# Optimization experiments

Measured on AMD Instinct MI355X. Metric: run time of the kernel, lower is better.

The kernel has to match this reference:

```python
import jax, jax.numpy as jnp
import numpy as np

HIDDEN = 64
DEPTH = 4  # 4 tanh layers + final linear


def _mlp(x, Ws, bs):
    # x: [..., 3] -> [..., 1]; weights stored as (in, out)
    h = x
    for W, b in zip(Ws[:-1], bs[:-1]):
        h = jnp.tanh(h @ W + b)
    return h @ Ws[-1] + bs[-1]


def setup_inputs() -> dict:
    key = jax.random.key(0)
    N = 262144
    dims = [3, HIDDEN, HIDDEN, HIDDEN, HIDDEN, 1]
    ks = jax.random.split(key, 2 * len(dims) + 3)
    inp = {}
    inp["x_data"] = jax.random.normal(ks[0], (N, 3), dtype=jnp.float32)
    inp["y_data"] = jax.random.normal(ks[1], (N, 1), dtype=jnp.float32)
    inp["x_phys"] = jax.random.normal(ks[2], (N, 3), dtype=jnp.float32)
    for i in range(5):
        fan_in = dims[i]
        bound = 1.0 / np.sqrt(fan_in)
        inp[f"W{i}"] = jax.random.uniform(ks[3 + 2 * i], (dims[i], dims[i + 1]),
                                          minval=-bound, maxval=bound, dtype=jnp.float32)
        inp[f"b{i}"] = jax.random.uniform(ks[4 + 2 * i], (dims[i + 1],),
                                          minval=-bound, maxval=bound, dtype=jnp.float32)
    inp["log_lambda"] = jnp.array([-2.0], dtype=jnp.float32)
    inp["log_alpha"] = jnp.array([-4.0], dtype=jnp.float32)
    return inp


def reference(x_data, y_data, x_phys,
              W0, b0, W1, b1, W2, b2, W3, b3, W4, b4,
              log_lambda, log_alpha):
    Ws = (W0, W1, W2, W3, W4)
    bs = (b0, b1, b2, b3, b4)
    alpha = jnp.exp(log_alpha)[0]
    lam = jnp.exp(log_lambda)[0]

    # data loss
    y_pred = _mlp(x_data, Ws, bs)  # [N,1]
    data_loss = jnp.mean((y_pred - y_data) ** 2)

    # PDE residual: dT/dt - alpha * (d2T/dx2 + d2T/dy2)
    def scalar_net(x):  # x: [3] -> scalar
        return _mlp(x, Ws, bs)[0]

    g = jax.grad(scalar_net)
    grads = jax.vmap(g)(x_phys)  # [N,3]
    dT_dt = grads[:, 2]

    e0 = jnp.array([1.0, 0.0, 0.0], dtype=x_phys.dtype)
    e1 = jnp.array([0.0, 1.0, 0.0], dtype=x_phys.dtype)

    def second_xy(x):
        # forward-over-reverse: Hessian columns for x and y directions
        _, hx = jax.jvp(g, (x,), (e0,))
        _, hy = jax.jvp(g, (x,), (e1,))
        return hx[0], hy[1]

    d2T_dx2, d2T_dy2 = jax.vmap(second_xy)(x_phys)  # each [N]

    residual = dT_dt - alpha * (d2T_dx2 + d2T_dy2)
    pde_loss = jnp.mean(residual ** 2)
    total_loss = data_loss + lam * pde_loss
    return total_loss, data_loss, pde_loss, alpha, lam
```

## Files before the change

kernel.cpp:

```cpp
#include <hip/hip_runtime.h>
#include <math.h>

#define NSAMP 262144
#define NW 4
#define BLK 256
#define PB 1024
#define DB 512
#define GRID (PB + DB)

#define SB_MASK 0x120

typedef _Float16 f16x8 __attribute__((ext_vector_type(8)));
typedef _Float16 f16x4 __attribute__((ext_vector_type(4)));
typedef __fp16   fp16x2 __attribute__((ext_vector_type(2)));
typedef float    f32x4 __attribute__((ext_vector_type(4)));
typedef float    f32x2 __attribute__((ext_vector_type(2)));

#define NCH 4

#define TWO_LOG2E 2.8853900817779268f

__device__ __forceinline__ f32x2 lo2(f32x4 v) { return __builtin_shufflevector(v, v, 0, 1); }
__device__ __forceinline__ f32x2 hi2(f32x4 v) { return __builtin_shufflevector(v, v, 2, 3); }
__device__ __forceinline__ f32x2 splat2(float s) { f32x2 v; v.x = s; v.y = s; return v; }

__device__ __forceinline__ f32x2 fast_tanh2(f32x2 x) {
    f32x2 t = x * splat2(TWO_LOG2E);
    f32x2 e;
    e.x = __builtin_amdgcn_exp2f(t.x);
    e.y = __builtin_amdgcn_exp2f(t.y);
    f32x2 d = e + splat2(1.0f);
    f32x2 rc;
    rc.x = __builtin_amdgcn_rcpf(d.x);
    rc.y = __builtin_amdgcn_rcpf(d.y);
    return splat2(1.0f) - splat2(2.0f) * rc;
}

__device__ __forceinline__ void phys_half(f32x2 z0, f32x2 z1, f32x2 z2, f32x2 z3,
                                          f32x2 alpha2, f32x2 (&h)[NCH])
{
    f32x2 a    = fast_tanh2(z0);
    f32x2 ap   = splat2(1.0f) - a * a;
    f32x2 napp = (a * ap) * alpha2;
    h[0] = a;
    h[1] = ap * z1;
    h[2] = ap * z2;
    f32x2 s = z1 * z1 + z2 * z2;
    h[3] = ap * z3 + napp * s;
}

__device__ __forceinline__ f16x4 pkpair(f32x2 lo, f32x2 hi) {
    union { f16x4 v; fp16x2 h[2]; } u;
    u.h[0] = __builtin_amdgcn_cvt_pkrtz(lo.x, lo.y);
    u.h[1] = __builtin_amdgcn_cvt_pkrtz(hi.x, hi.y);
    return u.v;
}

__device__ __forceinline__ void set_half(f16x8& dst, f16x4 v, int hi) {
    if (hi == 0) { dst[0] = v[0]; dst[1] = v[1]; dst[2] = v[2]; dst[3] = v[3]; }
    else         { dst[4] = v[0]; dst[5] = v[1]; dst[6] = v[2]; dst[7] = v[3]; }
}

__device__ __forceinline__ double shfl_xor_d(double v, int m) {
    union { double d; int i[2]; } u; u.d = v;
    u.i[0] = __shfl_xor(u.i[0], m, 64);
    u.i[1] = __shfl_xor(u.i[1], m, 64);
    return u.d;
}

template<bool DATA>
__device__ __forceinline__ void pw(const f32x4* acc, f16x4* out, f32x2 alpha2)
{
    if (DATA) {
        #pragma unroll
        for (int c = 0; c < NCH; c++)
            out[c] = pkpair(fast_tanh2(lo2(acc[c])), fast_tanh2(hi2(acc[c])));
    } else {
        f32x2 hlo[NCH], hhi[NCH];
        phys_half(lo2(acc[0]), lo2(acc[1]), lo2(acc[2]), lo2(acc[3]), alpha2, hlo);
        phys_half(hi2(acc[0]), hi2(acc[1]), hi2(acc[2]), hi2(acc[3]), alpha2, hhi);
        #pragma unroll
        for (int c = 0; c < NCH; c++) out[c] = pkpair(hlo[c], hhi[c]);
    }
}

template<bool DATA>
__device__ __forceinline__ void layer_mfma(
    const _Float16* sWA, const float (*sB)[64],
    int l, int rt, int q, int n, const f16x8 (&bf)[NCH][2], f32x4 (&acc)[NCH])
{
    const f32x4 z4 = {0.f, 0.f, 0.f, 0.f};
    f16x8 a0k = *(const f16x8*)&sWA[((((l * 4 + rt) * 2 + 0) * 4 + q) * 16 + n) * 8];
    f16x8 a1k = *(const f16x8*)&sWA[((((l * 4 + rt) * 2 + 1) * 4 + q) * 16 + n) * 8];
    f32x4 bias = *(const f32x4*)&sB[l + 1][rt * 16 + q * 4];
    #pragma unroll
    for (int c = 0; c < NCH; c++) {
        f32x4 cin = (DATA || c == 0) ? bias : z4;
        acc[c] = __builtin_amdgcn_mfma_f32_16x16x32_f16(a0k, bf[c][0], cin, 0, 0, 0);
        acc[c] = __builtin_amdgcn_mfma_f32_16x16x32_f16(a1k, bf[c][1], acc[c], 0, 0, 0);
    }
}

template<bool DATA>
__device__ __forceinline__ void hidden_layer(
    const _Float16* sWA, const float (*sB)[64],
    int l, int q, int n, const f16x8 (&bin)[NCH][2], f16x8 (&bout)[NCH][2], f32x2 alpha2)
{
    #pragma unroll
    for (int rt = 0; rt < 4; rt++) {
        f32x4 acc[NCH];
        layer_mfma<DATA>(sWA, sB, l, rt, q, n, bin, acc);
        f16x4 t6[NCH];
        pw<DATA>(acc, t6, alpha2);
        #pragma unroll
        for (int c = 0; c < NCH; c++) set_half(bout[c][rt >> 1], t6[c], rt & 1);
        __builtin_amdgcn_sched_barrier(SB_MASK);
    }
}

template<bool DATA>
__device__ __forceinline__ double run_mode(
    const float* __restrict__ xd, const float* __restrict__ yd,
    const float* __restrict__ xp, float alpha,
    const _Float16* sWA, const f16x8 (&a0r)[4],
    const float (*sB)[64], const float* sW4, float b4,
    int q, int n, int wstart, int wstride)
{
    const f16x8 zf = {0, 0, 0, 0, 0, 0, 0, 0};
    const f32x4 z4 = {0.f, 0.f, 0.f, 0.f};
    const f32x2 alpha2 = splat2(2.0f * alpha);

    const int NIT = DATA ? (NSAMP / (16 * NCH)) : (NSAMP / 16);
    double dacc = 0.0;

    for (int it = wstart; it < NIT; it += wstride) {
        f16x8 bfA[NCH][2], bfB[NCH][2];
        {
            f16x8 b0f[NCH];
            #pragma unroll
            for (int c = 0; c < NCH; c++) b0f[c] = zf;
            if (DATA) {
                if (q == 0) {
                    #pragma unroll
                    for (int c = 0; c < NCH; c++) {
                        int s = it * (16 * NCH) + c * 16 + n;
                        b0f[c][0] = (_Float16)xd[s * 3 + 0];
                        b0f[c][1] = (_Float16)xd[s * 3 + 1];
                        b0f[c][2] = (_Float16)xd[s * 3 + 2];
                    }
                }
            } else {
                if (q == 0) {
                    int s = it * 16 + n;
                    b0f[0][0] = (_Float16)xp[s * 3 + 0];
                    b0f[0][1] = (_Float16)xp[s * 3 + 1];
                    b0f[0][2] = (_Float16)xp[s * 3 + 2];
                    b0f[1][0] = (_Float16)1.0f;
                    b0f[2][1] = (_Float16)1.0f;
                    b0f[3][2] = (_Float16)1.0f;
                }
            }
            #pragma unroll
            for (int rt = 0; rt < 4; rt++) {
                f32x4 bias = *(const f32x4*)&sB[0][rt * 16 + q * 4];
                f32x4 acc[NCH];
                if (DATA) {
                    #pragma unroll
                    for (int c = 0; c < NCH; c++)
                        acc[c] = __builtin_amdgcn_mfma_f32_16x16x32_f16(a0r[rt], b0f[c], bias, 0, 0, 0);
                } else {
                    acc[0] = __builtin_amdgcn_mfma_f32_16x16x32_f16(a0r[rt], b0f[0], bias, 0, 0, 0);
                    #pragma unroll
                    for (int c = 1; c < NCH; c++)
                        acc[c] = __builtin_amdgcn_mfma_f32_16x16x32_f16(a0r[rt], b0f[c], z4, 0, 0, 0);
                }
                f16x4 t6[NCH];
                pw<DATA>(acc, t6, alpha2);
                #pragma unroll
                for (int c = 0; c < NCH; c++) set_half(bfA[c][rt >> 1], t6[c], rt & 1);
                __builtin_amdgcn_sched_barrier(SB_MASK);
            }
        }

        hidden_layer<DATA>(sWA, sB, 0, q, n, bfA, bfB, alpha2);
        hidden_layer<DATA>(sWA, sB, 1, q, n, bfB, bfA, alpha2);

        f32x2 t2[NCH];
        #pragma unroll
        for (int c = 0; c < NCH; c++) t2[c] = splat2(0.f);
        f32x2 tr2 = splat2(0.f);
        #pragma unroll
        for (int rt = 0; rt < 4; rt++) {
            f32x4 acc[NCH];
            layer_mfma<DATA>(sWA, sB, 2, rt, q, n, bfA, acc);
            f32x4 w4v = *(const f32x4*)&sW4[rt * 16 + q * 4];
            f32x2 wlo = lo2(w4v), whi = hi2(w4v);
            if (DATA) {
                #pragma unroll
                for (int c = 0; c < NCH; c++) {
                    t2[c] = t2[c] + wlo * fast_tanh2(lo2(acc[c]));
                    t2[c] = t2[c] + whi * fast_tanh2(hi2(acc[c]));
                }
            } else {
                f32x2 hlo[NCH], hhi[NCH];
                phys_half(lo2(acc[0]), lo2(acc[1]), lo2(acc[2]), lo2(acc[3]), alpha2, hlo);
                phys_half(hi2(acc[0]), hi2(acc[1]), hi2(acc[2]), hi2(acc[3]), alpha2, hhi);
                tr2 = tr2 + wlo * hlo[3];
                tr2 = tr2 + whi * hhi[3];
            }
        }

        if (DATA) {
            float t[NCH];
            #pragma unroll
            for (int c = 0; c < NCH; c++) {
                t[c] = t2[c].x + t2[c].y;
                t[c] += __shfl_xor(t[c], 16, 64);
                t[c] += __shfl_xor(t[c], 32, 64);
            }
            if (q == 0) {
                #pragma unroll
                for (int c = 0; c < NCH; c++) {
                    int s = it * (16 * NCH) + c * 16 + n;
                    float d = t[c] + b4 - yd[s];
                    dacc += (double)d * (double)d;
                }
            }
        } else {
            float tr = tr2.x + tr2.y;
            tr += __shfl_xor(tr, 16, 64);
            tr += __shfl_xor(tr, 32, 64);
            if (q == 0) dacc += (double)tr * (double)tr;
        }
    }
    return dacc;
}

__global__ __launch_bounds__(BLK)
__attribute__((amdgpu_waves_per_eu(2, 6)))
void fused_kernel(
    const float* __restrict__ xd, const float* __restrict__ yd, const float* __restrict__ xp,
    const float* __restrict__ W0, const float* __restrict__ b0,
    const float* __restrict__ W1, const float* __restrict__ b1,
    const float* __restrict__ W2, const float* __restrict__ b2,
    const float* __restrict__ W3, const float* __restrict__ b3,
    const float* __restrict__ W4, const float* __restrict__ b4,
    const float* __restrict__ log_alpha,
    double* __restrict__ accg)
{
    __shared__ __align__(16) _Float16 sWA[3 * 4 * 2 * 4 * 16 * 8];
    __shared__ __align__(16) float sB[4][64];
    __shared__ __align__(16) float sW4s[64];
    __shared__ float sb4;
    __shared__ double sRed[NW];

    const int tid = threadIdx.x;
    for (int idx = tid; idx < 3 * 4096; idx += BLK) {
        int l = idx >> 12, rem = idx & 4095, k = rem >> 6, m = rem & 63;
        const float* Ws = (l == 0) ? W1 : (l == 1) ? W2 : W3;
        int pk_ = (2 * (k >> 5) + ((k >> 2) & 1)) * 16 + ((k >> 3) & 3) * 4 + (k & 3);
        int rt = m >> 4, mlo = m & 15, kt = k >> 5, qq = (k >> 3) & 3, j = k & 7;
        sWA[((((l * 4 + rt) * 2 + kt) * 4 + qq) * 16 + mlo) * 8 + j] = (_Float16)Ws[pk_ * 64 + m];
    }
    for (int i = tid; i < 64; i += BLK) {
        sB[0][i] = b0[i]; sB[1][i] = b1[i]; sB[2][i] = b2[i]; sB[3][i] = b3[i];
        sW4s[i] = W4[i];
    }
    if (tid == 0) sb4 = b4[0];

    const int wave = tid >> 6, lane = tid & 63;
    const int q = lane >> 4, n = lane & 15;
    const float alpha = __expf(log_alpha[0]);

    f16x8 a0r[4];
    #pragma unroll
    for (int rt = 0; rt < 4; rt++) {
        f16x8 v = {0, 0, 0, 0, 0, 0, 0, 0};
        if (q == 0) {
            v[0] = (_Float16)W0[0 * 64 + rt * 16 + n];
            v[1] = (_Float16)W0[1 * 64 + rt * 16 + n];
            v[2] = (_Float16)W0[2 * 64 + rt * 16 + n];
        }
        a0r[rt] = v;
    }
    __syncthreads();

    double dacc;
    if (blockIdx.x < PB) {
        int ws = blockIdx.x * NW + wave;
        dacc = run_mode<false>(xd, yd, xp, alpha, sWA, a0r, sB, sW4s, sb4,
                               q, n, ws, PB * NW);
    } else {
        int ws = (blockIdx.x - PB) * NW + wave;
        dacc = run_mode<true>(xd, yd, xp, alpha, sWA, a0r, sB, sW4s, sb4,
                              q, n, ws, DB * NW);
    }
    #pragma unroll
    for (int m = 1; m < 64; m <<= 1) dacc = dacc + shfl_xor_d(dacc, m);
    if (lane == 0) sRed[wave] = dacc;
    __syncthreads();
    if (tid == 0)
        accg[blockIdx.x] = sRed[0] + sRed[1] + sRed[2] + sRed[3];
}

__global__ void finalize_kernel(const double* __restrict__ ws,
                                const float* __restrict__ log_lambda,
                                const float* __restrict__ log_alpha,
                                float* __restrict__ out)
{
    __shared__ double sp[256], sd[256];
    int tid = threadIdx.x;
    double pd = 0.0, dd = 0.0;
    for (int i = tid; i < PB; i += 256) pd += ws[i];
    for (int i = PB + tid; i < GRID; i += 256) dd += ws[i];
    sp[tid] = pd; sd[tid] = dd;
    __syncthreads();
    for (int s = 128; s > 0; s >>= 1) {
        if (tid < s) { sp[tid] += sp[tid + s]; sd[tid] += sd[tid + s]; }
        __syncthreads();
    }
    if (tid == 0) {
        float pde_loss  = (float)(sp[0] / (double)NSAMP);
        float data_loss = (float)(sd[0] / (double)NSAMP);
        float alpha = expf(log_alpha[0]);
        float lam   = expf(log_lambda[0]);
        out[0] = data_loss + lam * pde_loss;
        out[1] = data_loss;
        out[2] = pde_loss;
        out[3] = alpha;
        out[4] = lam;
    }
}

extern "C" void kernel_launch(void* const* d_in, const int* in_sizes, int n_in,
                              void* d_out, int out_size, void* d_ws, size_t ws_size,
                              hipStream_t stream) {
    const float* xd = (const float*)d_in[0];
    const float* yd = (const float*)d_in[1];
    const float* xp = (const float*)d_in[2];
    const float* W0 = (const float*)d_in[3];
    const float* b0 = (const float*)d_in[4];
    const float* W1 = (const float*)d_in[5];
    const float* b1 = (const float*)d_in[6];
    const float* W2 = (const float*)d_in[7];
    const float* b2 = (const float*)d_in[8];
    const float* W3 = (const float*)d_in[9];
    const float* b3 = (const float*)d_in[10];
    const float* W4 = (const float*)d_in[11];
    const float* b4 = (const float*)d_in[12];
    const float* log_lambda = (const float*)d_in[13];
    const float* log_alpha  = (const float*)d_in[14];
    float* out = (float*)d_out;
    double* acc = (double*)d_ws;

    fused_kernel<<<GRID, BLK, 0, stream>>>(xd, yd, xp, W0, b0, W1, b1, W2, b2, W3, b3,
                                           W4, b4, log_alpha, acc);
    finalize_kernel<<<1, 256, 0, stream>>>(acc, log_lambda, log_alpha, out);
}
```

Measured before the change: 150.3 us.

## Run physics and data passes in every wave with larger blocks

Replaces the split of blocks into dedicated physics and data blocks with a uniform grid of 1024 blocks of 8 waves. Each wave now runs the physics pass and then the data pass. The data pass uses 2 chunks instead of 4 to cut register pressure, and per-block partial sums are written as interleaved pairs. This is meant to balance load across waves and raise occupancy. The cost is doubling the number of template instantiations in one kernel, which may raise register use, and fewer chunks per data iteration reduce MFMA batching.

Result: no change. 151.6 us (+0.8%).

```diff
diff --git a/kernel.cpp b/kernel.cpp
--- a/kernel.cpp
+++ b/kernel.cpp
@@ -2,11 +2,10 @@
 #include <math.h>
 
 #define NSAMP 262144
-#define NW 4
-#define BLK 256
-#define PB 1024
-#define DB 512
-#define GRID (PB + DB)
+#define NW 8
+#define BLK 512
+#define GRID 1024
+#define TOTW (GRID * NW)
 
 #define SB_MASK 0x120
 
@@ -16,7 +15,7 @@
 typedef float    f32x4 __attribute__((ext_vector_type(4)));
 typedef float    f32x2 __attribute__((ext_vector_type(2)));
 
-#define NCH 4
+#define PCH 4
 
 #define TWO_LOG2E 2.8853900817779268f
 
@@ -37,7 +36,7 @@
 }
 
 __device__ __forceinline__ void phys_half(f32x2 z0, f32x2 z1, f32x2 z2, f32x2 z3,
-                                          f32x2 alpha2, f32x2 (&h)[NCH])
+                                          f32x2 alpha2, f32x2 (&h)[PCH])
 {
     f32x2 a    = fast_tanh2(z0);
     f32x2 ap   = splat2(1.0f) - a * a;
@@ -68,57 +67,57 @@
     return u.d;
 }
 
-template<bool DATA>
+template<bool DATA, int CH>
 __device__ __forceinline__ void pw(const f32x4* acc, f16x4* out, f32x2 alpha2)
 {
-    if (DATA) {
-        #pragma unroll
-        for (int c = 0; c < NCH; c++)
+    if constexpr (DATA) {
+        #pragma unroll
+        for (int c = 0; c < CH; c++)
             out[c] = pkpair(fast_tanh2(lo2(acc[c])), fast_tanh2(hi2(acc[c])));
     } else {
-        f32x2 hlo[NCH], hhi[NCH];
+        f32x2 hlo[PCH], hhi[PCH];
         phys_half(lo2(acc[0]), lo2(acc[1]), lo2(acc[2]), lo2(acc[3]), alpha2, hlo);
         phys_half(hi2(acc[0]), hi2(acc[1]), hi2(acc[2]), hi2(acc[3]), alpha2, hhi);
         #pragma unroll
-        for (int c = 0; c < NCH; c++) out[c] = pkpair(hlo[c], hhi[c]);
-    }
-}
-
-template<bool DATA>
+        for (int c = 0; c < CH; c++) out[c] = pkpair(hlo[c], hhi[c]);
+    }
+}
+
+template<bool DATA, int CH>
 __device__ __forceinline__ void layer_mfma(
     const _Float16* sWA, const float (*sB)[64],
-    int l, int rt, int q, int n, const f16x8 (&bf)[NCH][2], f32x4 (&acc)[NCH])
+    int l, int rt, int q, int n, const f16x8 (&bf)[CH][2], f32x4 (&acc)[CH])
 {
     const f32x4 z4 = {0.f, 0.f, 0.f, 0.f};
     f16x8 a0k = *(const f16x8*)&sWA[((((l * 4 + rt) * 2 + 0) * 4 + q) * 16 + n) * 8];
     f16x8 a1k = *(const f16x8*)&sWA[((((l * 4 + rt) * 2 + 1) * 4 + q) * 16 + n) * 8];
     f32x4 bias = *(const f32x4*)&sB[l + 1][rt * 16 + q * 4];
     #pragma unroll
-    for (int c = 0; c < NCH; c++) {
+    for (int c = 0; c < CH; c++) {
         f32x4 cin = (DATA || c == 0) ? bias : z4;
         acc[c] = __builtin_amdgcn_mfma_f32_16x16x32_f16(a0k, bf[c][0], cin, 0, 0, 0);
         acc[c] = __builtin_amdgcn_mfma_f32_16x16x32_f16(a1k, bf[c][1], acc[c], 0, 0, 0);
     }
 }
 
-template<bool DATA>
+template<bool DATA, int CH>
 __device__ __forceinline__ void hidden_layer(
     const _Float16* sWA, const float (*sB)[64],
-    int l, int q, int n, const f16x8 (&bin)[NCH][2], f16x8 (&bout)[NCH][2], f32x2 alpha2)
+    int l, int q, int n, const f16x8 (&bin)[CH][2], f16x8 (&bout)[CH][2], f32x2 alpha2)
 {
     #pragma unroll
     for (int rt = 0; rt < 4; rt++) {
-        f32x4 acc[NCH];
-        layer_mfma<DATA>(sWA, sB, l, rt, q, n, bin, acc);
-        f16x4 t6[NCH];
-        pw<DATA>(acc, t6, alpha2);
-        #pragma unroll
-        for (int c = 0; c < NCH; c++) set_half(bout[c][rt >> 1], t6[c], rt & 1);
+        f32x4 acc[CH];
+        layer_mfma<DATA, CH>(sWA, sB, l, rt, q, n, bin, acc);
+        f16x4 t6[CH];
+        pw<DATA, CH>(acc, t6, alpha2);
+        #pragma unroll
+        for (int c = 0; c < CH; c++) set_half(bout[c][rt >> 1], t6[c], rt & 1);
         __builtin_amdgcn_sched_barrier(SB_MASK);
     }
 }
 
-template<bool DATA>
+template<bool DATA, int CH>
 __device__ __forceinline__ double run_mode(
     const float* __restrict__ xd, const float* __restrict__ yd,
     const float* __restrict__ xp, float alpha,
@@ -130,20 +129,20 @@
     const f32x4 z4 = {0.f, 0.f, 0.f, 0.f};
     const f32x2 alpha2 = splat2(2.0f * alpha);
 
-    const int NIT = DATA ? (NSAMP / (16 * NCH)) : (NSAMP / 16);
+    const int NIT = DATA ? (NSAMP / (16 * CH)) : (NSAMP / 16);
     double dacc = 0.0;
 
     for (int it = wstart; it < NIT; it += wstride) {
-        f16x8 bfA[NCH][2], bfB[NCH][2];
+        f16x8 bfA[CH][2], bfB[CH][2];
         {
-            f16x8 b0f[NCH];
+            f16x8 b0f[CH];
             #pragma unroll
-            for (int c = 0; c < NCH; c++) b0f[c] = zf;
+            for (int c = 0; c < CH; c++) b0f[c] = zf;
             if (DATA) {
                 if (q == 0) {
                     #pragma unroll
-                    for (int c = 0; c < NCH; c++) {
-                        int s = it * (16 * NCH) + c * 16 + n;
+                    for (int c = 0; c < CH; c++) {
+                        int s = it * (16 * CH) + c * 16 + n;
                         b0f[c][0] = (_Float16)xd[s * 3 + 0];
                         b0f[c][1] = (_Float16)xd[s * 3 + 1];
                         b0f[c][2] = (_Float16)xd[s * 3 + 2];
@@ -163,46 +162,46 @@
             #pragma unroll
             for (int rt = 0; rt < 4; rt++) {
                 f32x4 bias = *(const f32x4*)&sB[0][rt * 16 + q * 4];
-                f32x4 acc[NCH];
+                f32x4 acc[CH];
                 if (DATA) {
                     #pragma unroll
-                    for (int c = 0; c < NCH; c++)
+                    for (int c = 0; c < CH; c++)
                         acc[c] = __builtin_amdgcn_mfma_f32_16x16x32_f16(a0r[rt], b0f[c], bias, 0, 0, 0);
                 } else {
                     acc[0] = __builtin_amdgcn_mfma_f32_16x16x32_f16(a0r[rt], b0f[0], bias, 0, 0, 0);
                     #pragma unroll
-                    for (int c = 1; c < NCH; c++)
+                    for (int c = 1; c < CH; c++)
                         acc[c] = __builtin_amdgcn_mfma_f32_16x16x32_f16(a0r[rt], b0f[c], z4, 0, 0, 0);
                 }
-                f16x4 t6[NCH];
-                pw<DATA>(acc, t6, alpha2);
+                f16x4 t6[CH];
+                pw<DATA, CH>(acc, t6, alpha2);
                 #pragma unroll
-                for (int c = 0; c < NCH; c++) set_half(bfA[c][rt >> 1], t6[c], rt & 1);
+                for (int c = 0; c < CH; c++) set_half(bfA[c][rt >> 1], t6[c], rt & 1);
                 __builtin_amdgcn_sched_barrier(SB_MASK);
             }
         }
 
-        hidden_layer<DATA>(sWA, sB, 0, q, n, bfA, bfB, alpha2);
-        hidden_layer<DATA>(sWA, sB, 1, q, n, bfB, bfA, alpha2);
-
-        f32x2 t2[NCH];
-        #pragma unroll
-        for (int c = 0; c < NCH; c++) t2[c] = splat2(0.f);
+        hidden_layer<DATA, CH>(sWA, sB, 0, q, n, bfA, bfB, alpha2);
+        hidden_layer<DATA, CH>(sWA, sB, 1, q, n, bfB, bfA, alpha2);
+
+        f32x2 t2[CH];
+        #pragma unroll
+        for (int c = 0; c < CH; c++) t2[c] = splat2(0.f);
         f32x2 tr2 = splat2(0.f);
         #pragma unroll
         for (int rt = 0; rt < 4; rt++) {
-            f32x4 acc[NCH];
-            layer_mfma<DATA>(sWA, sB, 2, rt, q, n, bfA, acc);
+            f32x4 acc[CH];
+            layer_mfma<DATA, CH>(sWA, sB, 2, rt, q, n, bfA, acc);
             f32x4 w4v = *(const f32x4*)&sW4[rt * 16 + q * 4];
             f32x2 wlo = lo2(w4v), whi = hi2(w4v);
             if (DATA) {
                 #pragma unroll
-                for (int c = 0; c < NCH; c++) {
+                for (int c = 0; c < CH; c++) {
                     t2[c] = t2[c] + wlo * fast_tanh2(lo2(acc[c]));
                     t2[c] = t2[c] + whi * fast_tanh2(hi2(acc[c]));
                 }
             } else {
-                f32x2 hlo[NCH], hhi[NCH];
+                f32x2 hlo[PCH], hhi[PCH];
                 phys_half(lo2(acc[0]), lo2(acc[1]), lo2(acc[2]), lo2(acc[3]), alpha2, hlo);
                 phys_half(hi2(acc[0]), hi2(acc[1]), hi2(acc[2]), hi2(acc[3]), alpha2, hhi);
                 tr2 = tr2 + wlo * hlo[3];
@@ -211,17 +210,17 @@
         }
 
         if (DATA) {
-            float t[NCH];
+            float t[CH];
             #pragma unroll
-            for (int c = 0; c < NCH; c++) {
+            for (int c = 0; c < CH; c++) {
                 t[c] = t2[c].x + t2[c].y;
                 t[c] += __shfl_xor(t[c], 16, 64);
                 t[c] += __shfl_xor(t[c], 32, 64);
             }
             if (q == 0) {
                 #pragma unroll
-                for (int c = 0; c < NCH; c++) {
-                    int s = it * (16 * NCH) + c * 16 + n;
+                for (int c = 0; c < CH; c++) {
+                    int s = it * (16 * CH) + c * 16 + n;
                     float d = t[c] + b4 - yd[s];
                     dacc += (double)d * (double)d;
                 }
@@ -237,7 +236,7 @@
 }
 
 __global__ __launch_bounds__(BLK)
-__attribute__((amdgpu_waves_per_eu(2, 6)))
+__attribute__((amdgpu_waves_per_eu(2, 8)))
 void fused_kernel(
     const float* __restrict__ xd, const float* __restrict__ yd, const float* __restrict__ xp,
     const float* __restrict__ W0, const float* __restrict__ b0,
@@ -252,7 +251,7 @@
     __shared__ __align__(16) float sB[4][64];
     __shared__ __align__(16) float sW4s[64];
     __shared__ float sb4;
-    __shared__ double sRed[NW];
+    __shared__ double sRedP[NW], sRedD[NW];
 
     const int tid = threadIdx.x;
     for (int idx = tid; idx < 3 * 4096; idx += BLK) {
@@ -285,22 +284,25 @@
     }
     __syncthreads();
 
-    double dacc;
-    if (blockIdx.x < PB) {
-        int ws = blockIdx.x * NW + wave;
-        dacc = run_mode<false>(xd, yd, xp, alpha, sWA, a0r, sB, sW4s, sb4,
-                               q, n, ws, PB * NW);
-    } else {
-        int ws = (blockIdx.x - PB) * NW + wave;
-        dacc = run_mode<true>(xd, yd, xp, alpha, sWA, a0r, sB, sW4s, sb4,
-                              q, n, ws, DB * NW);
-    }
+    const int wid = blockIdx.x * NW + wave;
+    double dp = run_mode<false, 4>(xd, yd, xp, alpha, sWA, a0r, sB, sW4s, sb4,
+                                   q, n, wid, TOTW);
+    double dd = run_mode<true, 2>(xd, yd, xp, alpha, sWA, a0r, sB, sW4s, sb4,
+                                  q, n, wid, TOTW);
     #pragma unroll
-    for (int m = 1; m < 64; m <<= 1) dacc = dacc + shfl_xor_d(dacc, m);
-    if (lane == 0) sRed[wave] = dacc;
+    for (int m = 1; m < 64; m <<= 1) {
+        dp = dp + shfl_xor_d(dp, m);
+        dd = dd + shfl_xor_d(dd, m);
+    }
+    if (lane == 0) { sRedP[wave] = dp; sRedD[wave] = dd; }
     __syncthreads();
-    if (tid == 0)
-        accg[blockIdx.x] = sRed[0] + sRed[1] + sRed[2] + sRed[3];
+    if (tid == 0) {
+        double sp = 0.0, sd = 0.0;
+        #pragma unroll
+        for (int w = 0; w < NW; w++) { sp += sRedP[w]; sd += sRedD[w]; }
+        accg[2 * blockIdx.x + 0] = sp;
+        accg[2 * blockIdx.x + 1] = sd;
+    }
 }
 
 __global__ void finalize_kernel(const double* __restrict__ ws,
@@ -311,8 +313,10 @@
     __shared__ double sp[256], sd[256];
     int tid = threadIdx.x;
     double pd = 0.0, dd = 0.0;
-    for (int i = tid; i < PB; i += 256) pd += ws[i];
-    for (int i = PB + tid; i < GRID; i += 256) dd += ws[i];
+    for (int i = tid; i < GRID; i += 256) {
+        pd += ws[2 * i + 0];
+        dd += ws[2 * i + 1];
+    }
     sp[tid] = pd; sd[tid] = dd;
     __syncthreads();
     for (int s = 128; s > 0; s >>= 1) {
```
